# Performance work log

Hardware: AMD Instinct MI355X
Metric: run time of the kernel (lower is better)

## Reference

```python
import jax, jax.numpy as jnp
import numpy as np

B, L, H, S, IN = 64, 64, 128, 64, 16  # batch, embedding_seq_len, hidden, seq_num, input_size


def setup_inputs() -> dict:
    key = jax.random.key(0)
    k = jax.random.split(key, 8)
    trip = jax.random.normal(k[0], (B, 256, IN), dtype=jnp.float32)
    valid_len = jax.random.randint(k[1], (B,), 0, 256)
    embedding = jax.random.normal(k[2], (B, L, H), dtype=jnp.float32)
    # gates: Linear(2H -> 4H), xavier-uniform weight
    lim_g = float(np.sqrt(6.0 / (2 * H + 4 * H)))
    W_gates = jax.random.uniform(k[3], (2 * H, 4 * H), minval=-lim_g, maxval=lim_g, dtype=jnp.float32)
    b_gates = jax.random.uniform(k[4], (4 * H,), minval=-1.0 / np.sqrt(2 * H), maxval=1.0 / np.sqrt(2 * H), dtype=jnp.float32)
    # linear: Linear(H -> input_size)
    lim_l = float(np.sqrt(6.0 / (H + IN)))
    W_lin = jax.random.uniform(k[5], (H, IN), minval=-lim_l, maxval=lim_l, dtype=jnp.float32)
    b_lin = jax.random.uniform(k[6], (IN,), minval=-1.0 / np.sqrt(H), maxval=1.0 / np.sqrt(H), dtype=jnp.float32)
    return {"trip": trip, "valid_len": valid_len, "embedding": embedding,
            "W_gates": W_gates, "b_gates": b_gates, "W_lin": W_lin, "b_lin": b_lin}


def _gate_update(inp, c, W_gates, b_gates):
    g = inp @ W_gates + b_gates
    f, i, o, cand = jnp.split(g, 4, axis=-1)
    c_new = jax.nn.sigmoid(f) * c + jax.nn.sigmoid(i) * jnp.tanh(cand)  # broadcasts [B,1,H] vs [B,L,H] at step 0
    h_new = jax.nn.sigmoid(o) * jnp.tanh(c_new)
    return c_new, h_new


def reference(trip, valid_len, embedding, W_gates, b_gates, W_lin, b_lin):
    x = trip  # sampler pass-through
    b, l, h = embedding.shape
    c0 = jnp.zeros((b, l, h), dtype=embedding.dtype)
    h0 = jnp.zeros((b, l, h), dtype=embedding.dtype)
    # step 0: gates on [embedding[:, :1], h[:, :1]] -> [B,1,4H], broadcast update
    inp0 = jnp.concatenate([embedding[:, :1, :], h0[:, :1, :]], axis=-1)
    c1, h1 = _gate_update(inp0, c0, W_gates, b_gates)

    def step(carry, _):
        c, hh = carry
        inp = jnp.concatenate([c, hh], axis=-1)  # [B,L,2H]
        c_new, h_new = _gate_update(inp, c, W_gates, b_gates)
        return (c_new, h_new), c_new

    (_, _), cs = jax.lax.scan(step, (c1, h1), None, length=S - 1)  # cs: [S-1,B,L,H]
    c_all = jnp.concatenate([c1[None], cs], axis=0)          # [S,B,L,H]
    c_all = jnp.transpose(c_all, (1, 0, 2, 3)).reshape(b, S * l, h)  # cat along dim=-2
    out = c_all @ W_lin + b_lin  # [B, S*L, IN]
    return (x, out)
```

## Files before the change

### kernel.cpp

```cpp
#include <hip/hip_runtime.h>

typedef _Float16 f16x8 __attribute__((ext_vector_type(8)));
typedef float f32x4 __attribute__((ext_vector_type(4)));

#define HDIM  128
#define NSTEP 64
#define NG    512
#define NBLK  8
#define BPB   8

#define LOG2E 1.44269504088896340736f

__device__ __forceinline__ float rcpf(float x) { return __builtin_amdgcn_rcpf(x); }
__device__ __forceinline__ float exp2neg(float x) {
    float r; asm("v_exp_f32 %0, -%1" : "=v"(r) : "v"(x)); return r;
}
__device__ __forceinline__ unsigned int packh2(float a, float b) {
    union { _Float16 h[2]; unsigned int u; } x;
    x.h[0] = (_Float16)a; x.h[1] = (_Float16)b; return x.u;
}

__global__ __launch_bounds__(512, 2) void recur_k(
    const float* __restrict__ emb, const float* __restrict__ Wg,
    const float* __restrict__ bg,  float* __restrict__ outb) {
    __shared__ __align__(16) unsigned int state_s[2][BPB * 128];

    const int blk = blockIdx.x, t = threadIdx.x;
    const int w = t >> 6, l = t & 63;
    const int lg = l >> 4, lr = l & 15;
    const int h = w * 16 + lr;
    const int mr = lr & 7;

    f16x8 B[4][8];
    f32x4 bias4[4];
    #pragma unroll
    for (int i = 0; i < 4; ++i) {
        const float sc = (i == 3) ? 2.f * LOG2E : LOG2E;
        const int c = i * 128 + h;
        const float bb = bg[c] * sc;
        bias4[i] = (f32x4){bb, bb, bb, bb};
        #pragma unroll
        for (int kt = 0; kt < 8; ++kt) {
            f16x8 v;
            #pragma unroll
            for (int e = 0; e < 8; ++e) {
                const int k = kt * 32 + lg * 8 + e;
                const int r = (k & 1) ? 128 + (k >> 1) : (k >> 1);
                v[e] = (_Float16)(Wg[r * NG + c] * sc);
            }
            B[i][kt] = v;
        }
    }
    #pragma unroll
    for (int i = 0; i < 4; ++i)
        #pragma unroll
        for (int kt = 0; kt < 8; ++kt)
            asm volatile("" : "+a"(B[i][kt]));

    for (int wd = t; wd < BPB * 128; wd += 512) {
        int batch = wd >> 7, kw = wd & 127;
        float ev = emb[(size_t)(blk * BPB + batch) * 64 * HDIM + kw];
        *(unsigned int*)((char*)state_s[0] + batch * 512 + ((kw * 4) ^ ((batch & 7) << 4)))
            = packh2(ev, 0.f);
    }

    const int b_base = (lg & 1) * 4 + (lg >> 1) * 2;
    const bool hi = (lg >= 2);
    float c2[2] = {0.f, 0.f};
    float ph2[2];
    int hoff[2];
    #pragma unroll
    for (int j = 0; j < 2; ++j)
        hoff[j] = (blk * BPB + b_base + j) * 65536 + h;
    __syncthreads();

    #pragma unroll 2
    for (int s = 0; s < NSTEP; ++s) {
        const char* buf = (const char*)state_s[s & 1];
        f16x8 a8[8];
        #pragma unroll
        for (int kt = 0; kt < 8; ++kt)
            a8[kt] = *(const f16x8*)(buf + mr * 512 + ((kt * 64 + lg * 16) ^ ((mr & 7) << 4)));
        if (s > 0) {
            float* ob = outb + (size_t)(s - 1) * 1024;
            #pragma unroll
            for (int j = 0; j < 2; ++j) ob[hoff[j]] = ph2[j];
        }
        f32x4 acc[4];
        #pragma unroll
        for (int i = 0; i < 4; ++i) acc[i] = bias4[i];
        asm volatile("s_nop 3");
        #pragma unroll
        for (int kt = 0; kt < 8; ++kt) {
            #pragma unroll
            for (int i = 0; i < 4; ++i)
                asm volatile("v_mfma_f32_16x16x32_f16 %0, %1, %2, %0"
                    : "+v"(acc[i]) : "v"(a8[kt]), "a"(B[i][kt]));
        }
        asm volatile("s_nop 7\n\ts_nop 7");
        __builtin_amdgcn_sched_barrier(0);
        char* bufn = (char*)state_s[(s + 1) & 1];
        #pragma unroll
        for (int j = 0; j < 2; ++j) {
            const int qa = hi ? 2 + j : j;
            float F = rcpf(1.f + exp2neg(acc[0][qa]));
            float I = rcpf(1.f + exp2neg(acc[1][qa]));
            float O = rcpf(1.f + exp2neg(acc[2][qa]));
            float Dd = fmaf(2.f, rcpf(1.f + exp2neg(acc[3][qa])), -1.f);
            float cn = fmaf(F, c2[j], I * Dd);
            float th = fmaf(2.f, rcpf(1.f + exp2neg(cn * (2.f * LOG2E))), -1.f);
            float hn = O * th;
            c2[j] = cn; ph2[j] = cn;
            const int batch = b_base + j;
            *(unsigned int*)(bufn + batch * 512 + ((4 * h) ^ ((batch & 7) << 4)))
                = packh2(cn, hn);
        }
        __syncthreads();
    }
    {
        float* ob = outb + (size_t)63 * 1024;
        #pragma unroll
        for (int j = 0; j < 2; ++j) ob[hoff[j]] = ph2[j];
    }
}

__global__ __launch_bounds__(256) void proj_expand_k(const float* __restrict__ Wl,
                                                     const float* __restrict__ bl,
                                                     const float* __restrict__ trip,
                                                     float* __restrict__ trip_out,
                                                     float* __restrict__ outb) {
    const int bs = blockIdx.x, t = threadIdx.x;
    if (bs >= 4096) {
        int i = (bs - 4096) * 256 + t;
        ((float4*)trip_out)[i] = ((const float4*)trip)[i];
        return;
    }
    __shared__ float c_s[HDIM];
    __shared__ __align__(16) float pj[16];
    float* reg = outb + (size_t)bs * 1024;
    if (t < HDIM) c_s[t] = reg[t];
    __syncthreads();
    if (t < 16) {
        float a = bl[t];
        #pragma unroll 16
        for (int h = 0; h < HDIM; ++h) a = fmaf(c_s[h], Wl[h * 16 + t], a);
        pj[t] = a;
    }
    __syncthreads();
    float4 v = ((const float4*)pj)[t & 3];
    ((float4*)reg)[t] = v;
}

extern "C" void kernel_launch(void* const* d_in, const int* in_sizes, int n_in,
                              void* d_out, int out_size, void* d_ws, size_t ws_size,
                              hipStream_t stream) {
    const float* trip = (const float*)d_in[0];
    const float* emb  = (const float*)d_in[2];
    const float* Wg   = (const float*)d_in[3];
    const float* bgp  = (const float*)d_in[4];
    const float* Wlp  = (const float*)d_in[5];
    const float* blp  = (const float*)d_in[6];
    float* out = (float*)d_out;

    recur_k<<<NBLK, 512, 0, stream>>>(emb, Wg, bgp, out + 262144);
    proj_expand_k<<<4096 + 256, 256, 0, stream>>>(Wlp, blp, trip, out, out + 262144);
}
```

Measured before the change: 76.31 us.

## Halve recurrence block to 4 waves, each wave computing 32 hidden columns

```diff
diff --git a/kernel.cpp b/kernel.cpp
--- a/kernel.cpp
+++ b/kernel.cpp
@@ -20,7 +20,7 @@
     x.h[0] = (_Float16)a; x.h[1] = (_Float16)b; return x.u;
 }
 
-__global__ __launch_bounds__(512, 2) void recur_k(
+__global__ __launch_bounds__(256, 1) void recur_k(
     const float* __restrict__ emb, const float* __restrict__ Wg,
     const float* __restrict__ bg,  float* __restrict__ outb) {
     __shared__ __align__(16) unsigned int state_s[2][BPB * 128];
@@ -28,17 +28,14 @@
     const int blk = blockIdx.x, t = threadIdx.x;
     const int w = t >> 6, l = t & 63;
     const int lg = l >> 4, lr = l & 15;
-    const int h = w * 16 + lr;
     const int mr = lr & 7;
 
-    f16x8 B[4][8];
-    f32x4 bias4[4];
+    f16x8 B[8][8];
     #pragma unroll
-    for (int i = 0; i < 4; ++i) {
-        const float sc = (i == 3) ? 2.f * LOG2E : LOG2E;
-        const int c = i * 128 + h;
-        const float bb = bg[c] * sc;
-        bias4[i] = (f32x4){bb, bb, bb, bb};
+    for (int i = 0; i < 8; ++i) {
+        const int g = i >> 1, hs = i & 1;
+        const float sc = (g == 3) ? 2.f * LOG2E : LOG2E;
+        const int c = g * 128 + w * 32 + hs * 16 + lr;
         #pragma unroll
         for (int kt = 0; kt < 8; ++kt) {
             f16x8 v;
@@ -52,29 +49,34 @@
         }
     }
     #pragma unroll
-    for (int i = 0; i < 4; ++i)
+    for (int i = 0; i < 8; ++i)
         #pragma unroll
         for (int kt = 0; kt < 8; ++kt)
             asm volatile("" : "+a"(B[i][kt]));
 
-    for (int wd = t; wd < BPB * 128; wd += 512) {
+    const int hs_own = lg >> 1;
+    const int b_base = (lg & 1) * 4;
+    const int h_upd = w * 32 + hs_own * 16 + lr;
+    const float bF = bg[0 * 128 + h_upd] * LOG2E;
+    const float bI = bg[1 * 128 + h_upd] * LOG2E;
+    const float bO = bg[2 * 128 + h_upd] * LOG2E;
+    const float bC = bg[3 * 128 + h_upd] * (2.f * LOG2E);
+
+    for (int wd = t; wd < BPB * 128; wd += 256) {
         int batch = wd >> 7, kw = wd & 127;
         float ev = emb[(size_t)(blk * BPB + batch) * 64 * HDIM + kw];
         *(unsigned int*)((char*)state_s[0] + batch * 512 + ((kw * 4) ^ ((batch & 7) << 4)))
             = packh2(ev, 0.f);
     }
 
-    const int b_base = (lg & 1) * 4 + (lg >> 1) * 2;
-    const bool hi = (lg >= 2);
-    float c2[2] = {0.f, 0.f};
-    float ph2[2];
-    int hoff[2];
+    float c4[4] = {0.f, 0.f, 0.f, 0.f};
+    float ph4[4];
+    int hoff[4];
     #pragma unroll
-    for (int j = 0; j < 2; ++j)
-        hoff[j] = (blk * BPB + b_base + j) * 65536 + h;
+    for (int q = 0; q < 4; ++q)
+        hoff[q] = (blk * BPB + b_base + q) * 65536 + h_upd;
     __syncthreads();
 
-    #pragma unroll 2
     for (int s = 0; s < NSTEP; ++s) {
         const char* buf = (const char*)state_s[s & 1];
         f16x8 a8[8];
@@ -84,16 +86,17 @@
         if (s > 0) {
             float* ob = outb + (size_t)(s - 1) * 1024;
             #pragma unroll
-            for (int j = 0; j < 2; ++j) ob[hoff[j]] = ph2[j];
+            for (int q = 0; q < 4; ++q) ob[hoff[q]] = ph4[q];
         }
-        f32x4 acc[4];
+        f32x4 acc[8];
         #pragma unroll
-        for (int i = 0; i < 4; ++i) acc[i] = bias4[i];
-        asm volatile("s_nop 3");
+        for (int i = 0; i < 8; ++i)
+            acc[i] = __builtin_amdgcn_mfma_f32_16x16x32_f16(
+                a8[0], B[i][0], (f32x4){0.f, 0.f, 0.f, 0.f}, 0, 0, 0);
         #pragma unroll
-        for (int kt = 0; kt < 8; ++kt) {
+        for (int kt = 1; kt < 8; ++kt) {
             #pragma unroll
-            for (int i = 0; i < 4; ++i)
+            for (int i = 0; i < 8; ++i)
                 asm volatile("v_mfma_f32_16x16x32_f16 %0, %1, %2, %0"
                     : "+v"(acc[i]) : "v"(a8[kt]), "a"(B[i][kt]));
         }
@@ -101,18 +104,17 @@
         __builtin_amdgcn_sched_barrier(0);
         char* bufn = (char*)state_s[(s + 1) & 1];
         #pragma unroll
-        for (int j = 0; j < 2; ++j) {
-            const int qa = hi ? 2 + j : j;
-            float F = rcpf(1.f + exp2neg(acc[0][qa]));
-            float I = rcpf(1.f + exp2neg(acc[1][qa]));
-            float O = rcpf(1.f + exp2neg(acc[2][qa]));
-            float Dd = fmaf(2.f, rcpf(1.f + exp2neg(acc[3][qa])), -1.f);
-            float cn = fmaf(F, c2[j], I * Dd);
+        for (int q = 0; q < 4; ++q) {
+            float F = rcpf(1.f + exp2neg(acc[0 + hs_own][q] + bF));
+            float I = rcpf(1.f + exp2neg(acc[2 + hs_own][q] + bI));
+            float O = rcpf(1.f + exp2neg(acc[4 + hs_own][q] + bO));
+            float Dd = fmaf(2.f, rcpf(1.f + exp2neg(acc[6 + hs_own][q] + bC)), -1.f);
+            float cn = fmaf(F, c4[q], I * Dd);
             float th = fmaf(2.f, rcpf(1.f + exp2neg(cn * (2.f * LOG2E))), -1.f);
             float hn = O * th;
-            c2[j] = cn; ph2[j] = cn;
-            const int batch = b_base + j;
-            *(unsigned int*)(bufn + batch * 512 + ((4 * h) ^ ((batch & 7) << 4)))
+            c4[q] = cn; ph4[q] = cn;
+            const int batch = b_base + q;
+            *(unsigned int*)(bufn + batch * 512 + ((4 * h_upd) ^ ((batch & 7) << 4)))
                 = packh2(cn, hn);
         }
         __syncthreads();
@@ -120,7 +122,7 @@
     {
         float* ob = outb + (size_t)63 * 1024;
         #pragma unroll
-        for (int j = 0; j < 2; ++j) ob[hoff[j]] = ph2[j];
+        for (int q = 0; q < 4; ++q) ob[hoff[q]] = ph4[q];
     }
 }
 
@@ -162,6 +164,6 @@
     const float* blp  = (const float*)d_in[6];
     float* out = (float*)d_out;
 
-    recur_k<<<NBLK, 512, 0, stream>>>(emb, Wg, bgp, out + 262144);
+    recur_k<<<NBLK, 256, 0, stream>>>(emb, Wg, bgp, out + 262144);
     proj_expand_k<<<4096 + 256, 256, 0, stream>>>(Wlp, blp, trip, out, out + 262144);
 }
```

Measured after the change: 202.3 us. +165.1%, slower.

## Split recurrence across 16 blocks of 4 batches each

Applied to the files above, without the earlier changes.

```diff
diff --git a/kernel.cpp b/kernel.cpp
--- a/kernel.cpp
+++ b/kernel.cpp
@@ -6,8 +6,8 @@
 #define HDIM  128
 #define NSTEP 64
 #define NG    512
-#define NBLK  8
-#define BPB   8
+#define NBLK  16
+#define BPB   4
 
 #define LOG2E 1.44269504088896340736f
 
@@ -28,17 +28,13 @@
     const int blk = blockIdx.x, t = threadIdx.x;
     const int w = t >> 6, l = t & 63;
     const int lg = l >> 4, lr = l & 15;
-    const int h = w * 16 + lr;
-    const int mr = lr & 7;
+    const int mr = lr & 3;
 
     f16x8 B[4][8];
-    f32x4 bias4[4];
     #pragma unroll
     for (int i = 0; i < 4; ++i) {
         const float sc = (i == 3) ? 2.f * LOG2E : LOG2E;
-        const int c = i * 128 + h;
-        const float bb = bg[c] * sc;
-        bias4[i] = (f32x4){bb, bb, bb, bb};
+        const int c = i * 128 + w * 16 + lr;
         #pragma unroll
         for (int kt = 0; kt < 8; ++kt) {
             f16x8 v;
@@ -57,6 +53,12 @@
         for (int kt = 0; kt < 8; ++kt)
             asm volatile("" : "+a"(B[i][kt]));
 
+    const int h_upd = w * 16 + lr;
+    const float bF = bg[0 * 128 + h_upd] * LOG2E;
+    const float bI = bg[1 * 128 + h_upd] * LOG2E;
+    const float bO = bg[2 * 128 + h_upd] * LOG2E;
+    const float bC = bg[3 * 128 + h_upd] * (2.f * LOG2E);
+
     for (int wd = t; wd < BPB * 128; wd += 512) {
         int batch = wd >> 7, kw = wd & 127;
         float ev = emb[(size_t)(blk * BPB + batch) * 64 * HDIM + kw];
@@ -64,34 +66,25 @@
             = packh2(ev, 0.f);
     }
 
-    const int b_base = (lg & 1) * 4 + (lg >> 1) * 2;
-    const bool hi = (lg >= 2);
-    float c2[2] = {0.f, 0.f};
-    float ph2[2];
-    int hoff[2];
-    #pragma unroll
-    for (int j = 0; j < 2; ++j)
-        hoff[j] = (blk * BPB + b_base + j) * 65536 + h;
+    float c1 = 0.f;
+    float ph1;
+    const int hoff = (blk * BPB + lg) * 65536 + h_upd;
     __syncthreads();
 
-    #pragma unroll 2
     for (int s = 0; s < NSTEP; ++s) {
         const char* buf = (const char*)state_s[s & 1];
         f16x8 a8[8];
         #pragma unroll
         for (int kt = 0; kt < 8; ++kt)
             a8[kt] = *(const f16x8*)(buf + mr * 512 + ((kt * 64 + lg * 16) ^ ((mr & 7) << 4)));
-        if (s > 0) {
-            float* ob = outb + (size_t)(s - 1) * 1024;
-            #pragma unroll
-            for (int j = 0; j < 2; ++j) ob[hoff[j]] = ph2[j];
-        }
+        if (s > 0) outb[(size_t)(s - 1) * 1024 + hoff] = ph1;
         f32x4 acc[4];
         #pragma unroll
-        for (int i = 0; i < 4; ++i) acc[i] = bias4[i];
-        asm volatile("s_nop 3");
+        for (int i = 0; i < 4; ++i)
+            acc[i] = __builtin_amdgcn_mfma_f32_16x16x32_f16(
+                a8[0], B[i][0], (f32x4){0.f, 0.f, 0.f, 0.f}, 0, 0, 0);
         #pragma unroll
-        for (int kt = 0; kt < 8; ++kt) {
+        for (int kt = 1; kt < 8; ++kt) {
             #pragma unroll
             for (int i = 0; i < 4; ++i)
                 asm volatile("v_mfma_f32_16x16x32_f16 %0, %1, %2, %0"
@@ -99,29 +92,22 @@
         }
         asm volatile("s_nop 7\n\ts_nop 7");
         __builtin_amdgcn_sched_barrier(0);
-        char* bufn = (char*)state_s[(s + 1) & 1];
-        #pragma unroll
-        for (int j = 0; j < 2; ++j) {
-            const int qa = hi ? 2 + j : j;
-            float F = rcpf(1.f + exp2neg(acc[0][qa]));
-            float I = rcpf(1.f + exp2neg(acc[1][qa]));
-            float O = rcpf(1.f + exp2neg(acc[2][qa]));
-            float Dd = fmaf(2.f, rcpf(1.f + exp2neg(acc[3][qa])), -1.f);
-            float cn = fmaf(F, c2[j], I * Dd);
+        {
+            float F = rcpf(1.f + exp2neg(acc[0][lg] + bF));
+            float I = rcpf(1.f + exp2neg(acc[1][lg] + bI));
+            float O = rcpf(1.f + exp2neg(acc[2][lg] + bO));
+            float Dd = fmaf(2.f, rcpf(1.f + exp2neg(acc[3][lg] + bC)), -1.f);
+            float cn = fmaf(F, c1, I * Dd);
             float th = fmaf(2.f, rcpf(1.f + exp2neg(cn * (2.f * LOG2E))), -1.f);
             float hn = O * th;
-            c2[j] = cn; ph2[j] = cn;
-            const int batch = b_base + j;
-            *(unsigned int*)(bufn + batch * 512 + ((4 * h) ^ ((batch & 7) << 4)))
+            c1 = cn; ph1 = cn;
+            char* bufn = (char*)state_s[(s + 1) & 1];
+            *(unsigned int*)(bufn + lg * 512 + ((4 * h_upd) ^ ((lg & 7) << 4)))
                 = packh2(cn, hn);
         }
         __syncthreads();
     }
-    {
-        float* ob = outb + (size_t)63 * 1024;
-        #pragma unroll
-        for (int j = 0; j < 2; ++j) ob[hoff[j]] = ph2[j];
-    }
+    outb[(size_t)63 * 1024 + hoff] = ph1;
 }
 
 __global__ __launch_bounds__(256) void proj_expand_k(const float* __restrict__ Wl,
```

After: 76.82 us. About the same (+0.7%).
